# Kernel optimization log

Hardware: AMD Instinct MI355X
Metric: run time of the kernel (lower is better)

Reference implementation:

```python
import jax, jax.numpy as jnp
import numpy as np
import math

B, IN, D, H, DEPTH, E, K = 16384, 128, 512, 8, 3, 8, 2
FF, EH = 4 * D, 256          # ffn width = 4*d_model; expert hidden fixed at 256 in source
EPSILON = 0.1                # forward() default epsilon (exploration mixing)
LN_EPS = 1e-5


def _ln(x, w, b):
    m = x.mean(-1, keepdims=True)
    v = x.var(-1, keepdims=True)  # biased variance, matching nn.LayerNorm
    return (x - m) / jnp.sqrt(v + LN_EPS) * w + b


def setup_inputs() -> dict:
    key = jax.random.key(0)
    ks = jax.random.split(key, 16)
    s = 0.02
    rn = lambda k, shape: jax.random.normal(k, shape, jnp.float32) * s
    return dict(
        x=jax.random.normal(ks[0], (B, IN), jnp.float32),
        embed_w=rn(ks[1], (IN, D)), embed_b=jnp.zeros((D,), jnp.float32),
        ln1_w=jnp.ones((DEPTH, D), jnp.float32), ln1_b=jnp.zeros((DEPTH, D), jnp.float32),
        inproj_w=rn(ks[2], (DEPTH, 3 * D, D)), inproj_b=jnp.zeros((DEPTH, 3 * D), jnp.float32),
        outproj_w=rn(ks[3], (DEPTH, D, D)), outproj_b=jnp.zeros((DEPTH, D), jnp.float32),
        ln2_w=jnp.ones((DEPTH, D), jnp.float32), ln2_b=jnp.zeros((DEPTH, D), jnp.float32),
        ffn_w1=rn(ks[4], (DEPTH, D, FF)), ffn_b1=jnp.zeros((DEPTH, FF), jnp.float32),
        ffn_w2=rn(ks[5], (DEPTH, FF, D)), ffn_b2=jnp.zeros((DEPTH, D), jnp.float32),
        router_w=rn(ks[6], (D, E)), router_b=jnp.zeros((E,), jnp.float32),
        exp_w1=rn(ks[7], (E, D, EH)), exp_b1=jnp.zeros((E, EH), jnp.float32),
        exp_w2=rn(ks[8], (E, EH, D)), exp_b2=jnp.zeros((E, D), jnp.float32),
        head_ln_w=jnp.ones((D,), jnp.float32), head_ln_b=jnp.zeros((D,), jnp.float32),
        head_w=rn(ks[9], (D, 1)), head_b=jnp.zeros((1,), jnp.float32),
    )


def reference(x, embed_w, embed_b, ln1_w, ln1_b, inproj_w, inproj_b,
              outproj_w, outproj_b, ln2_w, ln2_b, ffn_w1, ffn_b1, ffn_w2, ffn_b2,
              router_w, router_b, exp_w1, exp_b1, exp_w2, exp_b2,
              head_ln_w, head_ln_b, head_w, head_b):
    h = x @ embed_w + embed_b                       # [B, D]; unsqueeze(1) -> seq_len == 1
    for l in range(DEPTH):
        g = _ln(h, ln1_w[l], ln1_b[l])
        qkv = g @ inproj_w[l].T + inproj_b[l]       # [B, 3D]
        # seq_len == 1: softmax over the single key is exactly 1, so attn(h,h,h) == out_proj(V)
        v = qkv[:, 2 * D:]
        a = v @ outproj_w[l].T + outproj_b[l]
        h = h + a
        g = _ln(h, ln2_w[l], ln2_b[l])
        h = h + jax.nn.gelu(g @ ffn_w1[l] + ffn_b1[l], approximate=False) @ ffn_w2[l] + ffn_b2[l]
    z = h                                           # squeeze(1)

    # WaggleGate
    logits = z @ router_w + router_b                # [B, E]
    probs = jax.nn.softmax(logits, axis=-1)
    probs = (1.0 - EPSILON) * probs + EPSILON / E
    wts, idx = jax.lax.top_k(probs, K)              # [B, K]
    load = probs.mean(0)
    aux = (load * jnp.log(load * E + 1e-9)).sum() / math.log(E + 1e-9)

    # dense all-expert compute + sparse top-k combine (same math as per-sample dispatch)
    hmid = jax.nn.gelu(jnp.einsum('bd,edh->ebh', z, exp_w1) + exp_b1[:, None, :], approximate=False)
    eo = jnp.einsum('ebh,ehd->ebd', hmid, exp_w2) + exp_b2[:, None, :]   # [E, B, D]
    gate = jnp.zeros((z.shape[0], E), z.dtype).at[
        jnp.arange(z.shape[0])[:, None], idx].add(wts)                    # [B, E]
    moe = jnp.einsum('be,ebd->bd', gate, eo)

    z = z + moe
    logit = (_ln(z, head_ln_w, head_ln_b) @ head_w + head_b)[:, 0]       # [B]
    return logit, aux
```

## Files before the change

### kernel.cpp

```cpp
#include <hip/hip_runtime.h>
#include <hip/hip_bf16.h>

#define B_TOK 16384
#define IN_DIM 128
#define D_DIM 512
#define DEPTH 3
#define NEXP 8
#define FF_DIM 2048
#define EH_DIM 256
#define MAXSLOT 34816
#define MAXT256 136
#define NHBLK 64

typedef __attribute__((ext_vector_type(8))) __bf16 bf16x8;
typedef __attribute__((ext_vector_type(4))) float f32x4;
typedef __attribute__((ext_vector_type(4))) unsigned short u16x4;
typedef __attribute__((ext_vector_type(8))) unsigned short u16x8;

__device__ __forceinline__ unsigned short f2bf(float f){
    unsigned int u = __float_as_uint(f);
    u += 0x7fffu + ((u >> 16) & 1u);
    return (unsigned short)(u >> 16);
}
__device__ __forceinline__ float bf2f(unsigned short u){
    return __uint_as_float(((unsigned int)u) << 16);
}
__device__ __forceinline__ float geluf(float x){
    float x2 = x * x;
    float y  = x * (0.79788456080287f + 0.03567740814183f * x2);
    y = fminf(fmaxf(y, -15.0f), 15.0f);
    float e = __expf(2.0f * y);
    float th = 1.0f - 2.0f / (e + 1.0f);
    return 0.5f * x * (1.0f + th);
}
__device__ __forceinline__ void gload_lds16(const void* g, void* l){
    __builtin_amdgcn_global_load_lds((const __attribute__((address_space(1))) unsigned int*)g,
                                     (__attribute__((address_space(3))) unsigned int*)l,
                                     16, 0, 0);
}
__device__ __forceinline__ int xcd_swizzle(int orig, int nwg){
    const int q = nwg >> 3, r = nwg & 7;
    const int xcd = orig & 7;
    const int idx = orig >> 3;
    return (xcd < r ? xcd*(q+1) : r*(q+1) + (xcd-r)*q) + idx;
}

__global__ void zero_kernel(int* a, int na, int* b, int nb){
    const int i = blockIdx.x * blockDim.x + threadIdx.x;
    if (i < na) a[i] = 0;
    if (i < nb) b[i] = 0;
}

struct ConvSeg { const float* src; unsigned short* dst; int n4; };
struct ConvArgs { ConvSeg seg[2]; };

__global__ void convert_kernel(ConvArgs a){
    const int stride = gridDim.x * blockDim.x;
    const int tid = blockIdx.x * blockDim.x + threadIdx.x;
    for (int s = 0; s < 2; ++s){
        const f32x4* src = (const f32x4*)a.seg[s].src;
        u16x4* dst = (u16x4*)a.seg[s].dst;
        const int n4 = a.seg[s].n4;
        for (int i = tid; i < n4; i += stride){
            f32x4 v = src[i];
            u16x4 o;
            o[0] = f2bf(v[0]); o[1] = f2bf(v[1]); o[2] = f2bf(v[2]); o[3] = f2bf(v[3]);
            dst[i] = o;
        }
    }
}

struct TSeg { const float* src; unsigned short* dst; int K; int N; int tileStart; };
struct TArgs { TSeg seg[26]; };

__global__ void transpose_kernel(TArgs a){
    __shared__ float t[32][33];
    const int tile = blockIdx.x;
    int s = 0;
    #pragma unroll 1
    while (s < 25 && tile >= a.seg[s+1].tileStart) ++s;
    const TSeg sg = a.seg[s];
    const int local = tile - sg.tileStart;
    const int tilesN = sg.N >> 5;
    const int k0 = (local / tilesN) << 5;
    const int n0 = (local % tilesN) << 5;
    const int tx = threadIdx.x & 31;
    const int ty = threadIdx.x >> 5;
    #pragma unroll
    for (int j = 0; j < 4; ++j)
        t[ty + j*8][tx] = sg.src[(size_t)(k0 + ty + j*8) * sg.N + n0 + tx];
    __syncthreads();
    #pragma unroll
    for (int j = 0; j < 4; ++j){
        const int n = ty + j*8;
        sg.dst[(size_t)(n0 + n) * sg.K + k0 + tx] = f2bf(t[tx][n]);
    }
}

__global__ void foldb_kernel(const float* __restrict__ outproj_w, const float* __restrict__ outproj_b,
                             const float* __restrict__ inproj_b, float* __restrict__ bfold){
    const int l = blockIdx.x, n = threadIdx.x;
    const float* Wo = outproj_w + ((size_t)l*D_DIM + n)*D_DIM;
    const float* bv = inproj_b + l*3*D_DIM + 2*D_DIM;
    float acc = outproj_b[l*D_DIM + n];
    for (int j = 0; j < D_DIM; ++j) acc += Wo[j]*bv[j];
    bfold[l*D_DIM + n] = acc;
}

__global__ void __launch_bounds__(256, 2)
gemm_bt(const unsigned short* __restrict__ A, const unsigned short* __restrict__ Bt,
        const float* __restrict__ bias, unsigned short* __restrict__ out, int NB, int N, int K)
{
    __shared__ unsigned short sh[32768];
    const int nwg = gridDim.x;
    const int wg  = xcd_swizzle(blockIdx.x, nwg);
    const int bn  = wg % NB;
    const int bm  = wg / NB;

    const int tid  = threadIdx.x;
    const int lane = tid & 63;
    const int wave = tid >> 6;
    const int wm = (wave >> 1) << 6;
    const int wn = (wave & 1) << 6;

    f32x4 acc[4][4] = {};

    const unsigned short* Abase = A + (size_t)bm * 128 * K;
    const unsigned short* Bbase = Bt + (size_t)bn * 128 * K;
    const int soff = tid * 16;

    auto STAGE = [&](int b, int kt){
        char* Ab = (char*)(sh + b*16384);
        char* Bb = (char*)(sh + b*16384 + 8192);
        #pragma unroll
        for (int s = 0; s < 4; ++s){
            const int off = s*4096 + soff;
            const int row = off >> 7, colb = off & 127;
            gload_lds16((const char*)(Abase + (size_t)row*K + kt) + colb, Ab + off);
        }
        #pragma unroll
        for (int s = 0; s < 4; ++s){
            const int off = s*4096 + soff;
            const int row = off >> 7, colb = off & 127;
            gload_lds16((const char*)(Bbase + (size_t)row*K + kt) + colb, Bb + off);
        }
    };
    auto COMPUTE = [&](int b){
        const unsigned short* Ab = sh + b*16384;
        const unsigned short* Bb = sh + b*16384 + 8192;
        #pragma unroll
        for (int ks = 0; ks < 2; ++ks){
            const int k0 = ks*32 + ((lane>>4)<<3);
            bf16x8 af[4], bfr[4];
            #pragma unroll
            for (int i=0;i<4;i++) af[i]  = *(const bf16x8*)&Ab[(wm + i*16 + (lane&15))*64 + k0];
            #pragma unroll
            for (int j=0;j<4;j++) bfr[j] = *(const bf16x8*)&Bb[(wn + j*16 + (lane&15))*64 + k0];
            #pragma unroll
            for (int i=0;i<4;i++)
                #pragma unroll
                for (int j=0;j<4;j++)
                    acc[i][j] = __builtin_amdgcn_mfma_f32_16x16x32_bf16(af[i], bfr[j], acc[i][j], 0, 0, 0);
        }
    };

    STAGE(0, 0);
    __syncthreads();
    const int nk = K >> 6;
    int cur = 0;
    for (int i = 0; i < nk; ++i){
        if (i + 1 < nk) STAGE(cur ^ 1, (i + 1) << 6);
        COMPUTE(cur);
        __syncthreads();
        cur ^= 1;
    }

    const int r0 = ((lane>>4)<<2);
    const int cc = lane & 15;
    unsigned short* Ct = sh;
    float bcol[4];
    #pragma unroll
    for (int j=0;j<4;j++) bcol[j] = bias[bn*128 + wn + j*16 + cc];
    #pragma unroll
    for (int i=0;i<4;i++)
        #pragma unroll
        for (int r=0;r<4;r++){
            const int rl = wm + i*16 + r0 + r;
            #pragma unroll
            for (int j=0;j<4;j++)
                Ct[rl*128 + wn + j*16 + cc] = f2bf(acc[i][j][r] + bcol[j]);
        }
    __syncthreads();
    const int orow = tid >> 4;
    const int ocol = (tid & 15) * 8;
    #pragma unroll
    for (int p = 0; p < 8; ++p){
        const int row = p*16 + orow;
        *(u16x8*)(&out[(size_t)(bm*128 + row)*N + bn*128 + ocol]) = *(u16x8*)&Ct[row*128 + ocol];
    }
}

__global__ void __launch_bounds__(512, 2)
gemm256sq(const unsigned short* __restrict__ A, const unsigned short* __restrict__ Bt,
          const float* __restrict__ bias, unsigned short* __restrict__ out,
          int NB, int N, int K)
{
    __shared__ __align__(16) char sh[131072];
    const int nwg = gridDim.x;
    const int wg  = xcd_swizzle(blockIdx.x, nwg);
    const int bn  = wg % NB;
    const int bm  = wg / NB;
    const int m0  = bm * 256;
    const int n0  = bn * 256;

    const int tid = threadIdx.x, lane = tid & 63, wave = tid >> 6;
    const int wr = wave >> 2;
    const int wc = wave & 3;

    const int srow = wave*16 + (lane >> 3);
    const int scol = ((lane & 7) ^ (lane >> 3)) * 8;
    const unsigned short* aptr[2][2];
    const unsigned short* bptr[2][2];
    #pragma unroll
    for (int u = 0; u < 2; ++u)
        #pragma unroll
        for (int l = 0; l < 2; ++l){
            aptr[u][l] = A  + (size_t)(m0 + u*128 + srow + l*8) * K + scol;
            bptr[u][l] = Bt + (size_t)(n0 + u*128 + srow + l*8) * K + scol;
        }
    const int sdst = wave*2048 + lane*16;

    int ch[2];
    #pragma unroll
    for (int ks = 0; ks < 2; ++ks)
        ch[ks] = ((((ks<<2) + (lane>>4)) ^ (lane & 7)) << 4);
    const int arow = wr*128 + (lane & 15);
    const int brow = wc*64  + (lane & 15);

    f32x4 acc[8][4] = {};

    auto STAGE = [&](int buf, int kt){
        #pragma unroll
        for (int u = 0; u < 2; ++u)
            #pragma unroll
            for (int l = 0; l < 2; ++l)
                gload_lds16(aptr[u][l] + kt, sh + buf*32768 + u*16384 + l*1024 + sdst);
        #pragma unroll
        for (int u = 0; u < 2; ++u)
            #pragma unroll
            for (int l = 0; l < 2; ++l)
                gload_lds16(bptr[u][l] + kt, sh + 65536 + buf*32768 + u*16384 + l*1024 + sdst);
    };
    auto COMPUTE = [&](int buf){
        bf16x8 bfr[4][2];
        #pragma unroll
        for (int nf = 0; nf < 4; ++nf)
            #pragma unroll
            for (int ks = 0; ks < 2; ++ks)
                bfr[nf][ks] = *(const bf16x8*)(sh + 65536 + buf*32768 + (brow + nf*16)*128 + ch[ks]);
        #pragma unroll
        for (int mf = 0; mf < 8; ++mf){
            bf16x8 af[2];
            #pragma unroll
            for (int ks = 0; ks < 2; ++ks)
                af[ks] = *(const bf16x8*)(sh + buf*32768 + (arow + mf*16)*128 + ch[ks]);
            #pragma unroll
            for (int nf = 0; nf < 4; ++nf)
                #pragma unroll
                for (int ks = 0; ks < 2; ++ks)
                    acc[mf][nf] = __builtin_amdgcn_mfma_f32_16x16x32_bf16(af[ks], bfr[nf][ks], acc[mf][nf], 0,0,0);
        }
    };

    STAGE(0, 0);
    __syncthreads();
    const int nk = K >> 6;
    int cur = 0;
    for (int i = 0; i < nk; ++i){
        if (i + 1 < nk) STAGE(cur ^ 1, (i + 1) << 6);
        COMPUTE(cur);
        __syncthreads();
        cur ^= 1;
    }

    unsigned short* Ct = (unsigned short*)sh;
    const int r4 = (lane >> 4) * 4;
    const int cc = lane & 15;
    #pragma unroll
    for (int nf = 0; nf < 4; ++nf){
        const int col = wc*64 + nf*16 + cc;
        const float bv = bias[n0 + col];
        #pragma unroll
        for (int mf = 0; mf < 8; ++mf)
            #pragma unroll
            for (int r = 0; r < 4; ++r){
                const int row = wr*128 + mf*16 + r4 + r;
                Ct[row*256 + col] = f2bf(geluf(acc[mf][nf][r] + bv));
            }
    }
    __syncthreads();
    #pragma unroll
    for (int p = 0; p < 16; ++p){
        const int uidx = p*512 + tid;
        const int row = uidx >> 5;
        const int cu  = uidx & 31;
        *(u16x8*)(out + (size_t)(m0 + row)*N + n0 + cu*8) = *(const u16x8*)(Ct + row*256 + cu*8);
    }
}

#define G_GELU_BF16 0
#define G_BF16_RESID 1
#define G_GATED_BF16 2

template<int EPI, int MOE, int INDIRECT>
__global__ void __launch_bounds__(512, 2)
gemm256(const unsigned short* __restrict__ A, const unsigned short* __restrict__ BtG,
        const float* __restrict__ biasG, const unsigned short* __restrict__ resid,
        const int* __restrict__ tok, const int* __restrict__ offs,
        int wstride, int bstride, const float* __restrict__ gslot,
        unsigned short* __restrict__ out, int NB, int N, int K)
{
    __shared__ __align__(16) char sh[147456];
    const int nwg = gridDim.x;
    const int wg  = xcd_swizzle(blockIdx.x, nwg);
    const int bn  = wg % NB;
    const int bm  = wg / NB;
    const int m0  = bm * 256;

    const unsigned short* Bt = BtG;
    const float* bias = biasG;
    if (MOE){
        if (m0 >= offs[8]) return;
        int e = 0;
        #pragma unroll 1
        while (offs[e+1] <= m0) ++e;
        Bt   += (size_t)e * wstride;
        bias += (size_t)e * bstride;
    }

    const int tid = threadIdx.x, lane = tid & 63, wave = tid >> 6;
    const int wm = (wave >> 1) * 64;
    const int wn = (wave & 1) * 64;

    const int srow = wave*16 + (lane >> 3);
    const int scol = ((lane & 7) ^ (lane >> 3)) * 8;
    const unsigned short* aptr[2][2];
    #pragma unroll
    for (int u = 0; u < 2; ++u)
        #pragma unroll
        for (int l = 0; l < 2; ++l){
            const int r = u*128 + srow + l*8;
            const int gr = INDIRECT ? tok[m0 + r] : (m0 + r);
            aptr[u][l] = A + (size_t)gr * K + scol;
        }
    const unsigned short* bptr[2];
    #pragma unroll
    for (int l = 0; l < 2; ++l)
        bptr[l] = Bt + (size_t)(bn*128 + srow + l*8) * K + scol;
    const int sdst = wave*2048 + lane*16;

    int aoff[2], boff[2];
    #pragma unroll
    for (int ks = 0; ks < 2; ++ks){
        const int ch = (((ks<<2) + (lane>>4)) ^ (lane & 7)) << 4;
        aoff[ks] = (wm + (lane & 15))*128 + ch;
        boff[ks] = (wn + (lane & 15))*128 + ch;
    }

    f32x4 acc[4][4] = {};

    auto STAGE = [&](int buf, int kt){
        #pragma unroll
        for (int u = 0; u < 2; ++u)
            #pragma unroll
            for (int l = 0; l < 2; ++l)
                gload_lds16(aptr[u][l] + kt, sh + buf*32768 + u*16384 + l*1024 + sdst);
        #pragma unroll
        for (int l = 0; l < 2; ++l)
            gload_lds16(bptr[l] + kt, sh + 98304 + buf*16384 + l*1024 + sdst);
    };
    auto COMPUTE = [&](int buf){
        bf16x8 bfr[4][2];
        #pragma unroll
        for (int nf = 0; nf < 4; ++nf)
            #pragma unroll
            for (int ks = 0; ks < 2; ++ks)
                bfr[nf][ks] = *(const bf16x8*)(sh + 98304 + buf*16384 + nf*2048 + boff[ks]);
        #pragma unroll
        for (int mf = 0; mf < 4; ++mf){
            bf16x8 af[2];
            #pragma unroll
            for (int ks = 0; ks < 2; ++ks)
                af[ks] = *(const bf16x8*)(sh + buf*32768 + mf*2048 + aoff[ks]);
            #pragma unroll
            for (int nf = 0; nf < 4; ++nf)
                #pragma unroll
                for (int ks = 0; ks < 2; ++ks)
                    acc[mf][nf] = __builtin_amdgcn_mfma_f32_16x16x32_bf16(af[ks], bfr[nf][ks], acc[mf][nf], 0,0,0);
        }
    };

    STAGE(0, 0);
    __syncthreads();
    const int nk = K >> 6;
    int cur = 0;
    for (int i = 0; i < nk; ++i){
        if (i + 1 < nk) STAGE(cur ^ 1, (i + 1) << 6);
        COMPUTE(cur);
        __syncthreads();
        cur ^= 1;
    }

    const int r4 = (lane >> 4) * 4;
    const int cc = lane & 15;
    if (EPI == G_BF16_RESID){
        float* ctf = (float*)sh;
        #pragma unroll
        for (int nf = 0; nf < 4; ++nf){
            const float bv = bias[bn*128 + wn + nf*16 + cc];
            #pragma unroll
            for (int mf = 0; mf < 4; ++mf)
                #pragma unroll
                for (int r = 0; r < 4; ++r){
                    const int row = wm + mf*16 + r4 + r;
                    ctf[row*128 + wn + nf*16 + cc] = acc[mf][nf][r] + bv;
                }
        }
        __syncthreads();
        #pragma unroll
        for (int p = 0; p < 8; ++p){
            const int uidx = p*512 + tid;
            const int row = uidx >> 4;
            const int cu  = uidx & 15;
            const size_t gidx = (size_t)(m0 + row)*N + bn*128 + cu*8;
            u16x8 hv = *(const u16x8*)(resid + gidx);
            u16x8 o;
            #pragma unroll
            for (int j = 0; j < 8; ++j)
                o[j] = f2bf(bf2f(hv[j]) + ctf[row*128 + cu*8 + j]);
            *(u16x8*)(out + gidx) = o;
        }
    } else {
        unsigned short* ct = (unsigned short*)sh;
        #pragma unroll
        for (int nf = 0; nf < 4; ++nf){
            const float bv = bias[bn*128 + wn + nf*16 + cc];
            #pragma unroll
            for (int mf = 0; mf < 4; ++mf)
                #pragma unroll
                for (int r = 0; r < 4; ++r){
                    const int row = wm + mf*16 + r4 + r;
                    float v = acc[mf][nf][r] + bv;
                    if (EPI == G_GELU_BF16) v = geluf(v);
                    else                    v *= gslot[m0 + row];
                    ct[row*128 + wn + nf*16 + cc] = f2bf(v);
                }
        }
        __syncthreads();
        #pragma unroll
        for (int p = 0; p < 8; ++p){
            const int uidx = p*512 + tid;
            const int row = uidx >> 4;
            const int cu  = uidx & 15;
            *(u16x8*)(out + (size_t)(m0 + row)*N + bn*128 + cu*8) =
                *(const u16x8*)(ct + row*128 + cu*8);
        }
    }
}

__global__ void ln_kernel(const unsigned short* __restrict__ x, const float* __restrict__ w,
                          const float* __restrict__ b, unsigned short* __restrict__ out)
{
    const int lane = threadIdx.x & 63;
    const int wave = threadIdx.x >> 6;
    const int row  = blockIdx.x * 4 + wave;
    u16x8 hv = *(const u16x8*)(x + (size_t)row * D_DIM + lane*8);
    float v[8];
    #pragma unroll
    for (int j = 0; j < 8; ++j) v[j] = bf2f(hv[j]);
    float s = 0.f, s2 = 0.f;
    #pragma unroll
    for (int j = 0; j < 8; ++j){ s += v[j]; s2 += v[j]*v[j]; }
    #pragma unroll
    for (int o = 32; o > 0; o >>= 1){ s += __shfl_xor(s, o); s2 += __shfl_xor(s2, o); }
    const float mean = s * (1.0f/512.0f);
    const float var  = s2 * (1.0f/512.0f) - mean*mean;
    const float inv  = 1.0f / sqrtf(var + 1e-5f);
    const int k = lane*8;
    u16x8 o;
    #pragma unroll
    for (int j = 0; j < 8; ++j) o[j] = f2bf((v[j]-mean)*inv*w[k+j] + b[k+j]);
    *(u16x8*)(out + (size_t)row*D_DIM + k) = o;
}

__global__ void router_kernel(const unsigned short* __restrict__ z, const float* __restrict__ rw,
                              const float* __restrict__ rb,
                              int2* __restrict__ idx2, float2* __restrict__ wts2,
                              float* __restrict__ bsums)
{
    __shared__ float ps[4][8];
    const int lane = threadIdx.x & 63;
    const int wave = threadIdx.x >> 6;
    const int row  = blockIdx.x * 4 + wave;
    u16x8 hv = *(const u16x8*)(z + (size_t)row * D_DIM + lane*8);
    float acc[8] = {0,0,0,0,0,0,0,0};
    #pragma unroll
    for (int j = 0; j < 8; ++j){
        const float zv = bf2f(hv[j]);
        const float* wr = rw + (size_t)(lane*8 + j) * 8;
        f32x4 w0 = *(const f32x4*)wr;
        f32x4 w1 = *(const f32x4*)(wr + 4);
        acc[0] += zv*w0[0]; acc[1] += zv*w0[1]; acc[2] += zv*w0[2]; acc[3] += zv*w0[3];
        acc[4] += zv*w1[0]; acc[5] += zv*w1[1]; acc[6] += zv*w1[2]; acc[7] += zv*w1[3];
    }
    #pragma unroll
    for (int o = 32; o > 0; o >>= 1){
        #pragma unroll
        for (int e = 0; e < 8; ++e) acc[e] += __shfl_xor(acc[e], o);
    }
    if (lane == 0){
        float p[8]; float mx = -1e30f;
        #pragma unroll
        for (int e=0;e<8;e++){ p[e] = acc[e] + rb[e]; mx = fmaxf(mx, p[e]); }
        float se = 0.f;
        #pragma unroll
        for (int e=0;e<8;e++){ p[e] = expf(p[e]-mx); se += p[e]; }
        const float sc = 0.9f / se;
        #pragma unroll
        for (int e=0;e<8;e++) p[e] = p[e]*sc + 0.0125f;
        int i1 = 0;
        #pragma unroll
        for (int e=1;e<8;e++) if (p[e] > p[i1]) i1 = e;
        int i2 = (i1 == 0) ? 1 : 0;
        for (int e=i2+1;e<8;e++) if (e != i1 && p[e] > p[i2]) i2 = e;
        idx2[row] = make_int2(i1, i2);
        wts2[row] = make_float2(p[i1], p[i2]);
        #pragma unroll
        for (int e=0;e<8;e++) ps[wave][e] = p[e];
    }
    __syncthreads();
    if (threadIdx.x < 8){
        bsums[blockIdx.x*8 + threadIdx.x] =
            ps[0][threadIdx.x] + ps[1][threadIdx.x] + ps[2][threadIdx.x] + ps[3][threadIdx.x];
    }
}

__global__ void hist_kernel(const int2* __restrict__ idx2, int* __restrict__ blockHist){
    __shared__ int hc[8];
    if (threadIdx.x < 8) hc[threadIdx.x] = 0;
    __syncthreads();
    const int t = blockIdx.x * 256 + threadIdx.x;
    const int2 ii = idx2[t];
    atomicAdd(&hc[ii.x], 1);
    atomicAdd(&hc[ii.y], 1);
    __syncthreads();
    if (threadIdx.x < 8) blockHist[blockIdx.x*8 + threadIdx.x] = hc[threadIdx.x];
}

__global__ void scan_kernel(const int* __restrict__ blockHist, int* __restrict__ offs,
                            int* __restrict__ baseArr){
    if (threadIdx.x == 0){
        int counts[8];
        #pragma unroll
        for (int e=0;e<8;e++) counts[e] = 0;
        for (int b=0;b<NHBLK;b++)
            #pragma unroll
            for (int e=0;e<8;e++) counts[e] += blockHist[b*8+e];
        int o = 0; offs[0] = 0;
        int start[8];
        #pragma unroll
        for (int e=0;e<8;e++){ start[e] = o; o += (counts[e]+255)&~255; offs[e+1] = o; }
        for (int e=0;e<8;e++){
            int cur = start[e];
            for (int b=0;b<NHBLK;b++){ baseArr[b*8+e] = cur; cur += blockHist[b*8+e]; }
        }
    }
}

__global__ void assign_kernel(const int2* __restrict__ idx2, const float2* __restrict__ wts2,
                              const int* __restrict__ baseArr, int2* __restrict__ slot_map,
                              float* __restrict__ gslot, int* __restrict__ tok)
{
    __shared__ int cur[8];
    if (threadIdx.x < 8) cur[threadIdx.x] = 0;
    __syncthreads();
    const int t = blockIdx.x * 256 + threadIdx.x;
    const int2 ii = idx2[t];
    const float2 ww = wts2[t];
    const int r1 = atomicAdd(&cur[ii.x], 1);
    const int r2 = atomicAdd(&cur[ii.y], 1);
    const int s1 = baseArr[blockIdx.x*8 + ii.x] + r1;
    const int s2 = baseArr[blockIdx.x*8 + ii.y] + r2;
    slot_map[t] = make_int2(s1, s2);
    gslot[s1] = ww.x; gslot[s2] = ww.y;
    tok[s1] = t; tok[s2] = t;
}

__global__ void aux_kernel(const float* __restrict__ bsums, float* __restrict__ out_aux)
{
    __shared__ float part[256];
    const int t = threadIdx.x;
    const int e = t & 7, chunk = t >> 3;
    float s = 0.f;
    for (int blk = chunk*128; blk < chunk*128 + 128; ++blk) s += bsums[blk*8 + e];
    part[t] = s;
    __syncthreads();
    if (t < 8){
        float tot = 0.f;
        for (int c = 0; c < 32; ++c) tot += part[c*8 + t];
        part[t] = tot;
    }
    __syncthreads();
    if (t == 0){
        float aux = 0.f;
        for (int e2 = 0; e2 < 8; ++e2){
            float load = part[e2] * (1.0f/16384.0f);
            aux += load * logf(load * 8.0f + 1e-9f);
        }
        out_aux[0] = aux / 2.0794415416798357f;
    }
}

__global__ void head_kernel(const unsigned short* __restrict__ h, const unsigned short* __restrict__ eog,
                            const int2* __restrict__ slot_map,
                            const float* __restrict__ w, const float* __restrict__ b,
                            const float* __restrict__ hw, const float* __restrict__ hb,
                            float* __restrict__ out)
{
    const int lane = threadIdx.x & 63;
    const int wave = threadIdx.x >> 6;
    const int row  = blockIdx.x * 4 + wave;
    const int2 sm = slot_map[row];
    u16x8 hv = *(const u16x8*)(h + (size_t)row * D_DIM + lane*8);
    u16x8 e1 = *(const u16x8*)(eog + (size_t)sm.x * D_DIM + lane*8);
    u16x8 e2 = *(const u16x8*)(eog + (size_t)sm.y * D_DIM + lane*8);
    float v[8];
    #pragma unroll
    for (int j=0;j<8;j++) v[j] = bf2f(hv[j]) + bf2f(e1[j]) + bf2f(e2[j]);
    float s = 0.f, s2 = 0.f;
    #pragma unroll
    for (int j=0;j<8;j++){ s += v[j]; s2 += v[j]*v[j]; }
    #pragma unroll
    for (int o = 32; o > 0; o >>= 1){ s += __shfl_xor(s, o); s2 += __shfl_xor(s2, o); }
    const float mean = s * (1.0f/512.0f);
    const float var  = s2 * (1.0f/512.0f) - mean*mean;
    const float inv  = 1.0f / sqrtf(var + 1e-5f);
    const int k = lane*8;
    float dot = 0.f;
    #pragma unroll
    for (int j=0;j<8;j++) dot += ((v[j]-mean)*inv*w[k+j] + b[k+j]) * hw[k+j];
    #pragma unroll
    for (int o = 32; o > 0; o >>= 1) dot += __shfl_xor(dot, o);
    if (lane == 0) out[row] = dot + hb[0];
}

extern "C" void kernel_launch(void* const* d_in, const int* in_sizes, int n_in,
                              void* d_out, int out_size, void* d_ws, size_t ws_size,
                              hipStream_t stream)
{
    (void)in_sizes; (void)n_in; (void)out_size; (void)ws_size;
    const float* x         = (const float*)d_in[0];
    const float* embed_w   = (const float*)d_in[1];
    const float* embed_b   = (const float*)d_in[2];
    const float* ln1_w     = (const float*)d_in[3];
    const float* ln1_b     = (const float*)d_in[4];
    const float* inproj_w  = (const float*)d_in[5];
    const float* inproj_b  = (const float*)d_in[6];
    const float* outproj_w = (const float*)d_in[7];
    const float* outproj_b = (const float*)d_in[8];
    const float* ln2_w     = (const float*)d_in[9];
    const float* ln2_b     = (const float*)d_in[10];
    const float* ffn_w1    = (const float*)d_in[11];
    const float* ffn_b1    = (const float*)d_in[12];
    const float* ffn_w2    = (const float*)d_in[13];
    const float* ffn_b2    = (const float*)d_in[14];
    const float* router_w  = (const float*)d_in[15];
    const float* router_b  = (const float*)d_in[16];
    const float* exp_w1    = (const float*)d_in[17];
    const float* exp_b1    = (const float*)d_in[18];
    const float* exp_w2    = (const float*)d_in[19];
    const float* exp_b2    = (const float*)d_in[20];
    const float* head_ln_w = (const float*)d_in[21];
    const float* head_ln_b = (const float*)d_in[22];
    const float* head_w    = (const float*)d_in[23];
    const float* head_b    = (const float*)d_in[24];

    char* ws = (char*)d_ws;
    unsigned short* xbf   = (unsigned short*)(ws + 0);
    unsigned short* ebf   = (unsigned short*)(ws + 4194304);
    unsigned short* wobf  = (unsigned short*)(ws + 4325376);
    unsigned short* wvtbf = (unsigned short*)(ws + 5898240);
    unsigned short* wfold = (unsigned short*)(ws + 7471104);
    unsigned short* w1t   = (unsigned short*)(ws + 9043968);
    unsigned short* w2t   = (unsigned short*)(ws + 15335424);
    unsigned short* e1t   = (unsigned short*)(ws + 21626880);
    unsigned short* e2t   = (unsigned short*)(ws + 23724032);
    unsigned short* h     = (unsigned short*)(ws + 25821184);
    unsigned short* gbf   = (unsigned short*)(ws + 42598400);
    unsigned short* ubf   = (unsigned short*)(ws + 59375616);
    unsigned short* hmidg = ubf;
    unsigned short* eog   = (unsigned short*)(ws + 77201408);
    char* MISC = ws + 126484480;
    int*    offs     = (int*)(MISC + 0);
    float*  zbias    = (float*)(MISC + 256);
    float*  bfold    = (float*)(MISC + 2304);
    int2*   idx2     = (int2*)(MISC + 8448);
    float2* wts2     = (float2*)(MISC + 139520);
    int2*   slot_map = (int2*)(MISC + 270592);
    float*  gslot    = (float*)(MISC + 401664);
    int*    tok      = (int*)(MISC + 544768);
    float*  bsums    = (float*)(MISC + 684032);
    int*    blockHist= (int*)(MISC + 815104);
    int*    baseArr  = (int*)(MISC + 817152);
    float* out = (float*)d_out;

    zero_kernel<<<(MAXSLOT + 255)/256, 256, 0, stream>>>((int*)zbias, 512, tok, MAXSLOT);

    ConvArgs ca;
    ca.seg[0] = { x, xbf, B_TOK*IN_DIM/4 };
    ca.seg[1] = { outproj_w, wobf, DEPTH*D_DIM*D_DIM/4 };
    convert_kernel<<<1024, 256, 0, stream>>>(ca);

    TArgs ta;
    int tcur = 0, ti = 0;
    ta.seg[ti] = { embed_w, ebf, IN_DIM, D_DIM, tcur };
    tcur += (IN_DIM/32)*(D_DIM/32); ++ti;
    for (int l = 0; l < DEPTH; ++l){
        ta.seg[ti] = { ffn_w1 + (size_t)l*D_DIM*FF_DIM, w1t + (size_t)l*FF_DIM*D_DIM, D_DIM, FF_DIM, tcur };
        tcur += (D_DIM/32)*(FF_DIM/32); ++ti;
    }
    for (int l = 0; l < DEPTH; ++l){
        ta.seg[ti] = { ffn_w2 + (size_t)l*FF_DIM*D_DIM, w2t + (size_t)l*D_DIM*FF_DIM, FF_DIM, D_DIM, tcur };
        tcur += (FF_DIM/32)*(D_DIM/32); ++ti;
    }
    for (int e = 0; e < NEXP; ++e){
        ta.seg[ti] = { exp_w1 + (size_t)e*D_DIM*EH_DIM, e1t + (size_t)e*EH_DIM*D_DIM, D_DIM, EH_DIM, tcur };
        tcur += (D_DIM/32)*(EH_DIM/32); ++ti;
    }
    for (int e = 0; e < NEXP; ++e){
        ta.seg[ti] = { exp_w2 + (size_t)e*EH_DIM*D_DIM, e2t + (size_t)e*D_DIM*EH_DIM, EH_DIM, D_DIM, tcur };
        tcur += (EH_DIM/32)*(D_DIM/32); ++ti;
    }
    for (int l = 0; l < DEPTH; ++l){
        ta.seg[ti] = { inproj_w + (size_t)l*3*D_DIM*D_DIM + 2*D_DIM*D_DIM,
                       wvtbf + (size_t)l*D_DIM*D_DIM, D_DIM, D_DIM, tcur };
        tcur += (D_DIM/32)*(D_DIM/32); ++ti;
    }
    transpose_kernel<<<tcur, 256, 0, stream>>>(ta);

    foldb_kernel<<<DEPTH, D_DIM, 0, stream>>>(outproj_w, outproj_b, inproj_b, bfold);

    for (int l = 0; l < DEPTH; ++l){
        gemm_bt<<<16, 256, 0, stream>>>(
            wobf + (size_t)l*D_DIM*D_DIM, wvtbf + (size_t)l*D_DIM*D_DIM,
            zbias, wfold + (size_t)l*D_DIM*D_DIM, 4, D_DIM, D_DIM);
    }

    gemm_bt<<<(D_DIM/128)*(B_TOK/128), 256, 0, stream>>>(
        xbf, ebf, embed_b, h, D_DIM/128, D_DIM, IN_DIM);

    for (int l = 0; l < DEPTH; ++l){
        ln_kernel<<<B_TOK/4, 256, 0, stream>>>(h, ln1_w + l*D_DIM, ln1_b + l*D_DIM, gbf);
        gemm256<G_BF16_RESID,0,0><<<(B_TOK/256)*(D_DIM/128), 512, 0, stream>>>(
            gbf, wfold + (size_t)l*D_DIM*D_DIM, bfold + l*D_DIM, h,
            nullptr, nullptr, 0, 0, nullptr, h, D_DIM/128, D_DIM, D_DIM);
        ln_kernel<<<B_TOK/4, 256, 0, stream>>>(h, ln2_w + l*D_DIM, ln2_b + l*D_DIM, gbf);
        gemm256sq<<<(B_TOK/256)*(FF_DIM/256), 512, 0, stream>>>(
            gbf, w1t + (size_t)l*FF_DIM*D_DIM, ffn_b1 + l*FF_DIM, ubf, FF_DIM/256, FF_DIM, D_DIM);
        gemm256<G_BF16_RESID,0,0><<<(B_TOK/256)*(D_DIM/128), 512, 0, stream>>>(
            ubf, w2t + (size_t)l*D_DIM*FF_DIM, ffn_b2 + l*D_DIM, h,
            nullptr, nullptr, 0, 0, nullptr, h, D_DIM/128, D_DIM, FF_DIM);
    }

    router_kernel<<<B_TOK/4, 256, 0, stream>>>(h, router_w, router_b, idx2, wts2, bsums);
    aux_kernel<<<1, 256, 0, stream>>>(bsums, out + B_TOK);
    hist_kernel<<<NHBLK, 256, 0, stream>>>(idx2, blockHist);
    scan_kernel<<<1, 64, 0, stream>>>(blockHist, offs, baseArr);
    assign_kernel<<<B_TOK/256, 256, 0, stream>>>(idx2, wts2, baseArr, slot_map, gslot, tok);

    gemm256<G_GELU_BF16,1,1><<<MAXT256*(EH_DIM/128), 512, 0, stream>>>(
        h, e1t, exp_b1, nullptr, tok, offs, EH_DIM*D_DIM, EH_DIM, nullptr,
        hmidg, EH_DIM/128, EH_DIM, D_DIM);
    gemm256<G_GATED_BF16,1,0><<<MAXT256*(D_DIM/128), 512, 0, stream>>>(
        hmidg, e2t, exp_b2, nullptr, nullptr, offs, D_DIM*EH_DIM, D_DIM, gslot,
        eog, D_DIM/128, D_DIM, EH_DIM);

    head_kernel<<<B_TOK/4, 256, 0, stream>>>(h, eog, slot_map, head_ln_w, head_ln_b, head_w, head_b, out);
}
```

Before: 628.4 us.

## Interleave staged global-to-LDS loads with MFMA phases in 256x256 GEMM

Restructures the main loop of the 256x256 GEMM (used for the FFN up-projection with GELU) so that the next tile's loads are issued in four chunks, interleaved with four compute phases. Fine-grained vmcnt waits and raw s_barrier replace the single full __syncthreads per K step. It also raises wave priority around MFMA bursts with s_setprio. The aim is to hide global-to-LDS latency and reduce barrier stalls, at the cost of more barriers per iteration and fragile hand-counted vmcnt values.

```diff
diff --git a/kernel.cpp b/kernel.cpp
--- a/kernel.cpp
+++ b/kernel.cpp
@@ -43,6 +43,11 @@
     const int xcd = orig & 7;
     const int idx = orig >> 3;
     return (xcd < r ? xcd*(q+1) : r*(q+1) + (xcd-r)*q) + idx;
+}
+__device__ __forceinline__ void wgbar(){
+    asm volatile("" ::: "memory");
+    __builtin_amdgcn_s_barrier();
+    asm volatile("" ::: "memory");
 }
 
 __global__ void zero_kernel(int* a, int na, int* b, int nb){
@@ -217,18 +222,31 @@
     const int wr = wave >> 2;
     const int wc = wave & 3;
 
-    const int srow = wave*16 + (lane >> 3);
     const int scol = ((lane & 7) ^ (lane >> 3)) * 8;
-    const unsigned short* aptr[2][2];
-    const unsigned short* bptr[2][2];
-    #pragma unroll
-    for (int u = 0; u < 2; ++u)
-        #pragma unroll
-        for (int l = 0; l < 2; ++l){
-            aptr[u][l] = A  + (size_t)(m0 + u*128 + srow + l*8) * K + scol;
-            bptr[u][l] = Bt + (size_t)(n0 + u*128 + srow + l*8) * K + scol;
-        }
-    const int sdst = wave*2048 + lane*16;
+
+    const unsigned short* apt[2]; int adst[2];
+    const unsigned short* bpt[2]; int bdst[2];
+    #pragma unroll
+    for (int l = 0; l < 2; ++l){
+        const int idx  = wave*2 + l;
+        const int half = idx >> 3;
+        const int rb   = idx & 7;
+        apt[l]  = A  + (size_t)(m0 + half*128 + rb*8 + (lane>>3)) * K + scol;
+        adst[l] = half*16384 + rb*1024 + lane*16;
+        bpt[l]  = Bt + (size_t)(n0 + idx*8 + (lane>>3)) * K + scol;
+        bdst[l] = 65536 + idx*1024 + lane*16;
+    }
+
+    auto STA = [&](int buf, int unit, int kt){
+        #pragma unroll
+        for (int l = 0; l < 2; ++l)
+            gload_lds16(apt[l] + (size_t)unit*64*K + kt, sh + buf*32768 + adst[l] + unit*8192);
+    };
+    auto STB = [&](int buf, int u, int kt){
+        #pragma unroll
+        for (int l = 0; l < 2; ++l)
+            gload_lds16(bpt[l] + (size_t)u*128*K + kt, sh + buf*32768 + bdst[l] + u*16384);
+    };
 
     int ch[2];
     #pragma unroll
@@ -238,50 +256,107 @@
     const int brow = wc*64  + (lane & 15);
 
     f32x4 acc[8][4] = {};
-
-    auto STAGE = [&](int buf, int kt){
-        #pragma unroll
-        for (int u = 0; u < 2; ++u)
-            #pragma unroll
-            for (int l = 0; l < 2; ++l)
-                gload_lds16(aptr[u][l] + kt, sh + buf*32768 + u*16384 + l*1024 + sdst);
-        #pragma unroll
-        for (int u = 0; u < 2; ++u)
-            #pragma unroll
-            for (int l = 0; l < 2; ++l)
-                gload_lds16(bptr[u][l] + kt, sh + 65536 + buf*32768 + u*16384 + l*1024 + sdst);
-    };
-    auto COMPUTE = [&](int buf){
-        bf16x8 bfr[4][2];
+    bf16x8 bfr[4][2];
+
+    STB(0, 0, 0); STB(0, 1, 0); STA(0, 0, 0); STA(0, 1, 0);
+
+    const int nk = K >> 6;
+    for (int t = 0; t < nk; ++t){
+        const int buf = t & 1, nbuf = buf ^ 1;
+        const bool more = (t + 1) < nk;
+        const int ktn = (t + 1) << 6;
+
+        if (more) STB(nbuf, 0, ktn);
+        if (more) asm volatile("s_waitcnt vmcnt(4)" ::: "memory");
+        else      asm volatile("s_waitcnt vmcnt(2)" ::: "memory");
+        wgbar();
         #pragma unroll
         for (int nf = 0; nf < 4; ++nf)
             #pragma unroll
             for (int ks = 0; ks < 2; ++ks)
                 bfr[nf][ks] = *(const bf16x8*)(sh + 65536 + buf*32768 + (brow + nf*16)*128 + ch[ks]);
-        #pragma unroll
-        for (int mf = 0; mf < 8; ++mf){
-            bf16x8 af[2];
-            #pragma unroll
-            for (int ks = 0; ks < 2; ++ks)
-                af[ks] = *(const bf16x8*)(sh + buf*32768 + (arow + mf*16)*128 + ch[ks]);
-            #pragma unroll
-            for (int nf = 0; nf < 4; ++nf)
+        {
+            bf16x8 af[2][2];
+            #pragma unroll
+            for (int m2 = 0; m2 < 2; ++m2)
                 #pragma unroll
                 for (int ks = 0; ks < 2; ++ks)
-                    acc[mf][nf] = __builtin_amdgcn_mfma_f32_16x16x32_bf16(af[ks], bfr[nf][ks], acc[mf][nf], 0,0,0);
-        }
-    };
-
-    STAGE(0, 0);
-    __syncthreads();
-    const int nk = K >> 6;
-    int cur = 0;
-    for (int i = 0; i < nk; ++i){
-        if (i + 1 < nk) STAGE(cur ^ 1, (i + 1) << 6);
-        COMPUTE(cur);
-        __syncthreads();
-        cur ^= 1;
-    }
+                    af[m2][ks] = *(const bf16x8*)(sh + buf*32768 + (arow + (0+m2)*16)*128 + ch[ks]);
+            __builtin_amdgcn_s_setprio(1);
+            #pragma unroll
+            for (int m2 = 0; m2 < 2; ++m2)
+                #pragma unroll
+                for (int nf = 0; nf < 4; ++nf)
+                    #pragma unroll
+                    for (int ks = 0; ks < 2; ++ks)
+                        acc[0+m2][nf] = __builtin_amdgcn_mfma_f32_16x16x32_bf16(af[m2][ks], bfr[nf][ks], acc[0+m2][nf], 0,0,0);
+            __builtin_amdgcn_s_setprio(0);
+        }
+
+        if (more) STB(nbuf, 1, ktn);
+        wgbar();
+        {
+            bf16x8 af[2][2];
+            #pragma unroll
+            for (int m2 = 0; m2 < 2; ++m2)
+                #pragma unroll
+                for (int ks = 0; ks < 2; ++ks)
+                    af[m2][ks] = *(const bf16x8*)(sh + buf*32768 + (arow + (2+m2)*16)*128 + ch[ks]);
+            __builtin_amdgcn_s_setprio(1);
+            #pragma unroll
+            for (int m2 = 0; m2 < 2; ++m2)
+                #pragma unroll
+                for (int nf = 0; nf < 4; ++nf)
+                    #pragma unroll
+                    for (int ks = 0; ks < 2; ++ks)
+                        acc[2+m2][nf] = __builtin_amdgcn_mfma_f32_16x16x32_bf16(af[m2][ks], bfr[nf][ks], acc[2+m2][nf], 0,0,0);
+            __builtin_amdgcn_s_setprio(0);
+        }
+
+        if (more) STA(nbuf, 0, ktn);
+        if (more) asm volatile("s_waitcnt vmcnt(6)" ::: "memory");
+        else      asm volatile("s_waitcnt vmcnt(0)" ::: "memory");
+        wgbar();
+        {
+            bf16x8 af[2][2];
+            #pragma unroll
+            for (int m2 = 0; m2 < 2; ++m2)
+                #pragma unroll
+                for (int ks = 0; ks < 2; ++ks)
+                    af[m2][ks] = *(const bf16x8*)(sh + buf*32768 + (arow + (4+m2)*16)*128 + ch[ks]);
+            __builtin_amdgcn_s_setprio(1);
+            #pragma unroll
+            for (int m2 = 0; m2 < 2; ++m2)
+                #pragma unroll
+                for (int nf = 0; nf < 4; ++nf)
+                    #pragma unroll
+                    for (int ks = 0; ks < 2; ++ks)
+                        acc[4+m2][nf] = __builtin_amdgcn_mfma_f32_16x16x32_bf16(af[m2][ks], bfr[nf][ks], acc[4+m2][nf], 0,0,0);
+            __builtin_amdgcn_s_setprio(0);
+        }
+
+        if (more) STA(nbuf, 1, ktn);
+        wgbar();
+        {
+            bf16x8 af[2][2];
+            #pragma unroll
+            for (int m2 = 0; m2 < 2; ++m2)
+                #pragma unroll
+                for (int ks = 0; ks < 2; ++ks)
+                    af[m2][ks] = *(const bf16x8*)(sh + buf*32768 + (arow + (6+m2)*16)*128 + ch[ks]);
+            __builtin_amdgcn_s_setprio(1);
+            #pragma unroll
+            for (int m2 = 0; m2 < 2; ++m2)
+                #pragma unroll
+                for (int nf = 0; nf < 4; ++nf)
+                    #pragma unroll
+                    for (int ks = 0; ks < 2; ++ks)
+                        acc[6+m2][nf] = __builtin_amdgcn_mfma_f32_16x16x32_bf16(af[m2][ks], bfr[nf][ks], acc[6+m2][nf], 0,0,0);
+            __builtin_amdgcn_s_setprio(0);
+        }
+    }
+    asm volatile("s_waitcnt vmcnt(0)" ::: "memory");
+    wgbar();
 
     unsigned short* Ct = (unsigned short*)sh;
     const int r4 = (lane >> 4) * 4;
```

New measurement: 624.0 us. Within noise of the previous version (-0.7%).
